# Kernel tuning notes

Measured on AMD Instinct MI355X. Metric: run time of the kernel, lower is better.

The kernel has to match this reference:

```python
import jax, jax.numpy as jnp
import numpy as np

B, S, HID = 4, 1024, 1024
H = 16
D = HID // H  # 64
SPARSITY = 0.9  # keep prob = 0.1


def setup_inputs() -> dict:
    key = jax.random.key(0)
    ks = jax.random.split(key, 11)
    sc = 1.0 / np.sqrt(HID)
    x = jax.random.normal(ks[0], (B, S, HID), dtype=jnp.float32)
    Wq = jax.random.normal(ks[1], (HID, HID), dtype=jnp.float32) * sc
    bq = jnp.zeros((HID,), dtype=jnp.float32)
    Wk = jax.random.normal(ks[2], (HID, HID), dtype=jnp.float32) * sc
    bk = jnp.zeros((HID,), dtype=jnp.float32)
    Wv = jax.random.normal(ks[3], (HID, HID), dtype=jnp.float32) * sc
    bv = jnp.zeros((HID,), dtype=jnp.float32)
    Wo = jax.random.normal(ks[4], (HID, HID), dtype=jnp.float32) * sc
    bo = jnp.zeros((HID,), dtype=jnp.float32)
    temperature = jnp.ones((H, 1, 1), dtype=jnp.float32)
    # training-mode random sparsity mask: rand > sparsity -> keep (True)
    sparse_mask = jax.random.uniform(ks[5], (B, H, S, S)) > SPARSITY
    return {"x": x, "Wq": Wq, "bq": bq, "Wk": Wk, "bk": bk, "Wv": Wv,
            "bv": bv, "Wo": Wo, "bo": bo, "temperature": temperature,
            "sparse_mask": sparse_mask}


def reference(x, Wq, bq, Wk, bk, Wv, bv, Wo, bo, temperature, sparse_mask):
    b, s, _ = x.shape
    def split_heads(t):
        return t.reshape(b, s, H, D).transpose(0, 2, 1, 3)  # [B,H,S,D]
    q = split_heads(x @ Wq + bq)
    k = split_heads(x @ Wk + bk)
    v = split_heads(x @ Wv + bv)
    scores = jnp.einsum('bhqd,bhkd->bhqk', q, k) / np.sqrt(D)
    scores = scores * temperature  # [H,1,1] broadcasts over [B,H,S,S]
    scores = jnp.where(sparse_mask, scores, -jnp.inf)
    attn = jax.nn.softmax(scores, axis=-1)
    out = jnp.einsum('bhqk,bhkd->bhqd', attn, v)
    out = out.transpose(0, 2, 1, 3).reshape(b, s, HID)
    return out @ Wo + bo
```

## Files before the change

### kernel.cpp

```cpp
#include <hip/hip_runtime.h>

typedef unsigned short u16;
typedef short short8 __attribute__((ext_vector_type(8)));
typedef float f32x4 __attribute__((ext_vector_type(4)));
typedef float float4v __attribute__((ext_vector_type(4)));
typedef u16 u16x4 __attribute__((ext_vector_type(4)));
typedef unsigned uint2v __attribute__((ext_vector_type(2)));
typedef unsigned long long u64;

__device__ __forceinline__ u16 f2bf(float f) {
  union { float f; unsigned u; } v; v.f = f;
  unsigned r = v.u + 0x7FFFu + ((v.u >> 16) & 1u);
  return (u16)(r >> 16);
}

__device__ __forceinline__ unsigned cvtpk(float lo, float hi) {
  unsigned r;
  asm("v_cvt_pk_bf16_f32 %0, %1, %2" : "=v"(r) : "v"(lo), "v"(hi));
  return r;
}

__device__ __forceinline__ void gload16(const u16* g, u16* l) {
  __builtin_amdgcn_global_load_lds(
      (const __attribute__((address_space(1))) void*)g,
      (__attribute__((address_space(3))) void*)l, 16, 0, 0);
}

union PackSS { unsigned u[4]; short8 s; };

__global__ __launch_bounds__(256)
void prep_kernel(const void* __restrict__ mask, u64* __restrict__ bits,
                 const float* __restrict__ x, u16* __restrict__ xb,
                 const float* __restrict__ W0, const float* __restrict__ W1,
                 const float* __restrict__ W2, const float* __restrict__ W3,
                 u16* __restrict__ Wt) {
  __shared__ float t[32][33];
  __shared__ int sf;
  const int bid = blockIdx.x;
  if (bid < 4096) {
    if (threadIdx.x == 0) sf = 0;
    __syncthreads();
    {
      uint4 v = ((const uint4*)mask)[threadIdx.x];
      unsigned xs[4] = {v.x, v.y, v.z, v.w};
      int f = 0;
#pragma unroll
      for (int d = 0; d < 4; ++d) {
        unsigned u = xs[d];
        if (u == 0x3F800000u) f |= 1;
        if (u & 0xFFFFFF00u) f |= 2;
        if ((d & 1) && u) f |= 4;
      }
      if (f) atomicOr(&sf, f);
    }
    __syncthreads();
    const int fl = sf;
    const int fmt = (fl & 1) ? 2 : ((fl & 2) ? 0 : ((fl & 4) ? 1 : 3));

    const int wi = bid * 256 + threadIdx.x;
    u64 b = 0;
    if (fmt == 0) {
      const uint4* mp = (const uint4*)mask + (size_t)wi * 4;
#pragma unroll
      for (int i = 0; i < 4; ++i) {
        uint4 v = mp[i];
        unsigned xw[4] = {v.x, v.y, v.z, v.w};
#pragma unroll
        for (int d = 0; d < 4; ++d)
#pragma unroll
          for (int by = 0; by < 4; ++by)
            if (xw[d] & (0xFFu << (by * 8))) b |= 1ULL << (i * 16 + d * 4 + by);
      }
    } else if (fmt != 3) {
      const uint4* mp = (const uint4*)mask + (size_t)wi * 16;
#pragma unroll
      for (int i = 0; i < 16; ++i) {
        uint4 v = mp[i];
        if (v.x) b |= 1ULL << (i * 4 + 0);
        if (v.y) b |= 1ULL << (i * 4 + 1);
        if (v.z) b |= 1ULL << (i * 4 + 2);
        if (v.w) b |= 1ULL << (i * 4 + 3);
      }
    } else {
      const uint4* mp = (const uint4*)mask + (size_t)wi * 32;
#pragma unroll
      for (int i = 0; i < 32; ++i) {
        uint4 v = mp[i];
        if (v.x | v.y) b |= 1ULL << (i * 2 + 0);
        if (v.z | v.w) b |= 1ULL << (i * 2 + 1);
      }
    }
    int bh = wi >> 14, q = (wi >> 4) & 1023, kt = wi & 15;
    bits[((size_t)bh * 16 + kt) * 1024 + q] = b;
  } else if (bid < 8192) {
    int i = ((bid - 4096) * 256 + threadIdx.x) * 4;
    float4v v = *(const float4v*)(x + i);
    u16x4 o;
    o[0] = f2bf(v[0]); o[1] = f2bf(v[1]); o[2] = f2bf(v[2]); o[3] = f2bf(v[3]);
    *(u16x4*)(xb + i) = o;
  } else {
    int i = bid - 8192;
    int z = i >> 10, rest = i & 1023;
    const float* W = (z == 0) ? W0 : (z == 1) ? W1 : (z == 2) ? W2 : W3;
    u16* out = Wt + (size_t)z * 1024 * 1024;
    int n0 = (rest & 31) * 32, k0 = (rest >> 5) * 32;
    int tx = threadIdx.x & 31, ty = threadIdx.x >> 5;
#pragma unroll
    for (int j = 0; j < 4; ++j)
      t[ty + 8 * j][tx] = W[(size_t)(k0 + ty + 8 * j) * 1024 + n0 + tx];
    __syncthreads();
#pragma unroll
    for (int j = 0; j < 4; ++j)
      out[(size_t)(n0 + ty + 8 * j) * 1024 + k0 + tx] = f2bf(t[tx][ty + 8 * j]);
  }
}

template<int BN>
__global__ __launch_bounds__(256)
void gemm_kernel(const u16* __restrict__ A,
                 const u16* __restrict__ Bt0, const u16* __restrict__ Bt1, const u16* __restrict__ Bt2,
                 const float* __restrict__ b0, const float* __restrict__ b1, const float* __restrict__ b2,
                 const float* __restrict__ temp,
                 u16* __restrict__ qb, u16* __restrict__ kb, u16* __restrict__ vT,
                 float* __restrict__ fo, int phase) {
  constexpr int K = 1024;
  constexpr int WN = BN / 2;
  constexpr int NC = WN / 16;
  __shared__ u16 As[128 * 32];
  __shared__ u16 Bs[BN * 32];
  const int tid = threadIdx.x;
  const int lane = tid & 63, w = tid >> 6;
  const int l15 = lane & 15, l4 = lane >> 4;
  const int m0 = blockIdx.x * 128, n0 = blockIdx.y * BN;
  const int z = blockIdx.z;
  const u16* Bt = (z == 0) ? Bt0 : (z == 1) ? Bt1 : Bt2;
  const float* bias = (z == 0) ? b0 : (z == 1) ? b1 : b2;
  const int wr = w >> 1, wc = w & 1;

  f32x4 acc[4][NC] = {};

  const int c0 = tid, c1 = 256 + tid;
  const u16* ga0 = A + (size_t)(m0 + (c0 >> 2)) * K + (c0 & 3) * 8;
  const u16* ga1 = A + (size_t)(m0 + (c1 >> 2)) * K + (c1 & 3) * 8;
  const u16* gb0 = Bt + (size_t)(n0 + (c0 >> 2)) * K + (c0 & 3) * 8;
  const u16* gb1 = Bt + (size_t)(n0 + (c1 >> 2)) * K + (c1 & 3) * 8;
  u16* la0 = As + c0 * 8;
  u16* la1 = As + c1 * 8;
  u16* lb0 = Bs + c0 * 8;
  u16* lb1 = Bs + c1 * 8;

  for (int kt = 0; kt < K; kt += 32) {
    gload16(ga0 + kt, la0);
    gload16(ga1 + kt, la1);
    gload16(gb0 + kt, lb0);
    if (BN == 128) gload16(gb1 + kt, lb1);
    __syncthreads();
    short8 af[4], bfr[NC];
#pragma unroll
    for (int r = 0; r < 4; ++r)
      af[r] = *(const short8*)(As + (wr * 64 + r * 16 + l15) * 32 + l4 * 8);
#pragma unroll
    for (int c = 0; c < NC; ++c)
      bfr[c] = *(const short8*)(Bs + (wc * WN + c * 16 + l15) * 32 + l4 * 8);
#pragma unroll
    for (int r = 0; r < 4; ++r)
#pragma unroll
      for (int c = 0; c < NC; ++c)
        acc[r][c] = __builtin_amdgcn_mfma_f32_16x16x32_bf16(bfr[c], af[r], acc[r][c], 0, 0, 0);
    __syncthreads();
  }

  float bvj[NC][4];
#pragma unroll
  for (int c = 0; c < NC; ++c)
#pragma unroll
    for (int j = 0; j < 4; ++j)
      bvj[c][j] = bias[n0 + wc * WN + c * 16 + l4 * 4 + j];
  const float fac = (phase == 0 && z == 0)
      ? temp[(n0 + wc * WN) >> 6] * 0.18033688011112042f : 1.0f;

#pragma unroll
  for (int r = 0; r < 4; ++r) {
    const int mm = m0 + wr * 64 + r * 16 + l15;
    const int b = mm >> 10, s = mm & 1023;
#pragma unroll
    for (int c = 0; c < NC; ++c) {
      const int n = n0 + wc * WN + c * 16 + l4 * 4;
      if (phase == 1) {
        float4v o;
#pragma unroll
        for (int j = 0; j < 4; ++j) o[j] = acc[r][c][j] + bvj[c][j];
        *(float4v*)(fo + (size_t)mm * 1024 + n) = o;
      } else if (z == 2) {
#pragma unroll
        for (int j = 0; j < 4; ++j)
          vT[((size_t)b * 1024 + n + j) * 1024 + s] = f2bf(acc[r][c][j] + bvj[c][j]);
      } else {
        unsigned lo = cvtpk((acc[r][c][0] + bvj[c][0]) * fac, (acc[r][c][1] + bvj[c][1]) * fac);
        unsigned hi = cvtpk((acc[r][c][2] + bvj[c][2]) * fac, (acc[r][c][3] + bvj[c][3]) * fac);
        unsigned o2[2] = {lo, hi};
        int hh = n >> 6, d = n & 63;
        u16* dst = (z == 0) ? qb : kb;
        *(unsigned long long*)(dst + ((((size_t)b * 16 + hh) * 1024 + s) * 64 + d)) =
            *(unsigned long long*)o2;
      }
    }
  }
}

__global__ __launch_bounds__(512, 4)
void attn_kernel(const u16* __restrict__ qb, const u16* __restrict__ kb, const u16* __restrict__ vT,
                 const u64* __restrict__ mbits, u16* __restrict__ oh) {
  __shared__ u16 Ks[2][64 * 64];
  __shared__ u16 Vs[2][64 * 64];
  const int tid = threadIdx.x, lane = tid & 63, w = tid >> 6;
  const int l15 = lane & 15, l4 = lane >> 4;
  const int id = blockIdx.x;
  const int xcd = id & 7, sl = id >> 3;
  const int bh = xcd * 8 + (sl >> 3), qx = sl & 7;
  const int b = bh >> 4, h = bh & 15;
  const int q0 = qx * 128 + w * 16;
  const u16* qp = qb + ((size_t)bh * 1024 + q0) * 64;
  const u16* kp = kb + (size_t)bh * 1024 * 64;
  const u16* vp = vT + (size_t)bh * 64 * 1024;

  const int sr = tid >> 3, sc = ((tid & 7) ^ (sr & 7)) * 8;
  const int swz8 = (l15 & 7) << 3;
  const int vswz = l15 & 7;

  short8 qf0 = *(const short8*)(qp + (size_t)l15 * 64 + l4 * 8);
  short8 qf1 = *(const short8*)(qp + (size_t)l15 * 64 + 32 + l4 * 8);

  float m = -1e30f, l = 0.f;
  f32x4 oacc[4] = {};

  const u64* mb = mbits + (size_t)bh * 16 * 1024 + q0 + l15;
  u64 wcur = mb[0];

  gload16(kp + (size_t)sr * 64 + sc, &Ks[0][tid * 8]);
  gload16(vp + (size_t)sr * 1024 + sc, &Vs[0][tid * 8]);

  for (int t = 0; t < 16; ++t) {
    const int buf = t & 1;
    __syncthreads();

    if (t < 15) {
      const int k1 = (t + 1) * 64;
      gload16(kp + (size_t)(k1 + sr) * 64 + sc, &Ks[buf ^ 1][tid * 8]);
      gload16(vp + (size_t)sr * 1024 + k1 + sc, &Vs[buf ^ 1][tid * 8]);
    }
    u64 wnext = (t < 15) ? mb[(t + 1) * 1024] : 0ULL;

    f32x4 s[4] = {};
    __builtin_amdgcn_s_setprio(1);
#pragma unroll
    for (int cb = 0; cb < 4; ++cb) {
      const u16* kr = &Ks[buf][(cb * 16 + l15) * 64];
      short8 kf0 = *(const short8*)(kr + ((l4 * 8) ^ swz8));
      short8 kf1 = *(const short8*)(kr + ((32 + l4 * 8) ^ swz8));
      s[cb] = __builtin_amdgcn_mfma_f32_16x16x32_bf16(kf0, qf0, s[cb], 0, 0, 0);
      s[cb] = __builtin_amdgcn_mfma_f32_16x16x32_bf16(kf1, qf1, s[cb], 0, 0, 0);
    }
    __builtin_amdgcn_s_setprio(0);

    float mt = fmaxf(fmaxf(s[0][0], s[0][1]), fmaxf(s[0][2], s[0][3]));
#pragma unroll
    for (int cb = 1; cb < 4; ++cb)
      mt = fmaxf(mt, fmaxf(fmaxf(s[cb][0], s[cb][1]), fmaxf(s[cb][2], s[cb][3])));
    mt = fmaxf(mt, __shfl_xor(mt, 16));
    mt = fmaxf(mt, __shfl_xor(mt, 32));
    if (!__all(mt <= m + 8.f)) {
      float mnew = fmaxf(m, mt);
      float al = exp2f(m - mnew);
      l *= al;
#pragma unroll
      for (int db = 0; db < 4; ++db) oacc[db] *= al;
      m = mnew;
    }
    unsigned hws[4] = {(unsigned)wcur, (unsigned)(wcur >> 16),
                       (unsigned)(wcur >> 32), (unsigned)(wcur >> 48)};
    float rs = 0.f;
#pragma unroll
    for (int cb = 0; cb < 4; ++cb) {
#pragma unroll
      for (int j = 0; j < 4; ++j) {
        float p = exp2f(s[cb][j] - m);
        p = ((hws[cb] >> (l4 * 4 + j)) & 1) ? p : 0.f;
        rs += p;
        s[cb][j] = p;
      }
    }
    rs += __shfl_xor(rs, 16);
    rs += __shfl_xor(rs, 32);
    l += rs;

    PackSS pb0, pb1;
    pb0.u[0] = cvtpk(s[0][0], s[0][1]); pb0.u[1] = cvtpk(s[0][2], s[0][3]);
    pb0.u[2] = cvtpk(s[1][0], s[1][1]); pb0.u[3] = cvtpk(s[1][2], s[1][3]);
    pb1.u[0] = cvtpk(s[2][0], s[2][1]); pb1.u[1] = cvtpk(s[2][2], s[2][3]);
    pb1.u[2] = cvtpk(s[3][0], s[3][1]); pb1.u[3] = cvtpk(s[3][2], s[3][3]);

    __builtin_amdgcn_s_setprio(1);
#pragma unroll
    for (int kg = 0; kg < 2; ++kg) {
#pragma unroll
      for (int db = 0; db < 4; ++db) {
        const u16* vrow = &Vs[buf][(db * 16 + l15) * 64];
        const int e0 = (((4 * kg + (l4 >> 1)) ^ vswz) << 3) + (l4 & 1) * 4;
        const int e1 = (((4 * kg + 2 + (l4 >> 1)) ^ vswz) << 3) + (l4 & 1) * 4;
        uint2v v0 = *(const uint2v*)(vrow + e0);
        uint2v v1 = *(const uint2v*)(vrow + e1);
        PackSS vf;
        vf.u[0] = v0[0]; vf.u[1] = v0[1]; vf.u[2] = v1[0]; vf.u[3] = v1[1];
        oacc[db] = __builtin_amdgcn_mfma_f32_16x16x32_bf16(
            vf.s, kg ? pb1.s : pb0.s, oacc[db], 0, 0, 0);
      }
    }
    __builtin_amdgcn_s_setprio(0);
    wcur = wnext;
  }

  float rl = 1.f / l;
  u16* orow = oh + ((size_t)b * 1024 + q0 + l15) * 1024 + h * 64;
#pragma unroll
  for (int db = 0; db < 4; ++db) {
    unsigned a0 = cvtpk(oacc[db][0] * rl, oacc[db][1] * rl);
    unsigned a1 = cvtpk(oacc[db][2] * rl, oacc[db][3] * rl);
    unsigned oA[2] = {a0, a1};
    *(unsigned long long*)(orow + db * 16 + l4 * 4) = *(unsigned long long*)oA;
  }
}

extern "C" void kernel_launch(void* const* d_in, const int* in_sizes, int n_in,
                              void* d_out, int out_size, void* d_ws, size_t ws_size,
                              hipStream_t stream) {
  const float* x = (const float*)d_in[0];
  const float* Wq = (const float*)d_in[1];
  const float* bq = (const float*)d_in[2];
  const float* Wk = (const float*)d_in[3];
  const float* bk = (const float*)d_in[4];
  const float* Wv = (const float*)d_in[5];
  const float* bv = (const float*)d_in[6];
  const float* Wo = (const float*)d_in[7];
  const float* bo = (const float*)d_in[8];
  const float* temp = (const float*)d_in[9];
  const void* mask = (const void*)d_in[10];

  char* ws = (char*)d_ws;
  u16* xb = (u16*)(ws + 256);
  u16* Wt = xb + (size_t)4 * 1024 * 1024;
  u16* qbuf = Wt + (size_t)4 * 1024 * 1024;
  u16* kbuf = qbuf + (size_t)4 * 1024 * 1024;
  u16* vTb = kbuf + (size_t)4 * 1024 * 1024;
  u64* mbits = (u64*)(vTb + (size_t)4 * 1024 * 1024);
  u16* oh = xb;

  prep_kernel<<<12288, 256, 0, stream>>>(mask, mbits, x, xb, Wq, Wk, Wv, Wo, Wt);
  gemm_kernel<128><<<dim3(32, 8, 3), 256, 0, stream>>>(
      xb, Wt, Wt + 1024 * 1024, Wt + 2 * 1024 * 1024,
      bq, bk, bv, temp, qbuf, kbuf, vTb, nullptr, 0);
  attn_kernel<<<512, 512, 0, stream>>>(qbuf, kbuf, vTb, mbits, oh);
  gemm_kernel<64><<<dim3(32, 16, 1), 256, 0, stream>>>(
      oh, Wt + 3 * 1024 * 1024, nullptr, nullptr,
      bo, nullptr, nullptr, temp, nullptr, nullptr, nullptr, (float*)d_out, 1);
}
```

Baseline: 188.4 us.

## Process two 16-row query tiles per wave in attention to reuse K/V fragments

The attention kernel moves from 8 waves of 16 query rows each to 4 waves of 32 query rows each, with 256 threads per block. Each K fragment and V fragment read from LDS now feeds two MFMAs, one per query sub-tile, which halves LDS reads per unit of work and gives more independent MFMAs to interleave with softmax. Each thread now issues two async global-to-LDS loads per tile, and LDS offsets are precomputed outside the loop. The cost is roughly doubled accumulator and score registers per wave and fewer waves per block, which may reduce occupancy and latency hiding.

```diff
diff --git a/kernel.cpp b/kernel.cpp
--- a/kernel.cpp
+++ b/kernel.cpp
@@ -20,7 +20,7 @@
   return r;
 }
 
-__device__ __forceinline__ void gload16(const u16* g, u16* l) {
+__device__ __forceinline__ void gload16(const void* g, void* l) {
   __builtin_amdgcn_global_load_lds(
       (const __attribute__((address_space(1))) void*)g,
       (__attribute__((address_space(3))) void*)l, 16, 0, 0);
@@ -102,7 +102,7 @@
     int i = bid - 8192;
     int z = i >> 10, rest = i & 1023;
     const float* W = (z == 0) ? W0 : (z == 1) ? W1 : (z == 2) ? W2 : W3;
-    u16* out = Wt + (size_t)z * 1024 * 1024;
+    u16* out = Wt + (size_t)z * 1048576;
     int n0 = (rest & 31) * 32, k0 = (rest >> 5) * 32;
     int tx = threadIdx.x & 31, ty = threadIdx.x >> 5;
 #pragma unroll
@@ -208,37 +208,96 @@
   }
 }
 
-__global__ __launch_bounds__(512, 4)
-void attn_kernel(const u16* __restrict__ qb, const u16* __restrict__ kb, const u16* __restrict__ vT,
-                 const u64* __restrict__ mbits, u16* __restrict__ oh) {
+__device__ __forceinline__ void softmax_reg(f32x4* s, u64 wcur, float& m, float& l,
+                                            f32x4* oacc, int l4,
+                                            PackSS& p0, PackSS& p1) {
+  float mt = fmaxf(fmaxf(s[0][0], s[0][1]), fmaxf(s[0][2], s[0][3]));
+#pragma unroll
+  for (int cb = 1; cb < 4; ++cb)
+    mt = fmaxf(mt, fmaxf(fmaxf(s[cb][0], s[cb][1]), fmaxf(s[cb][2], s[cb][3])));
+  mt = fmaxf(mt, __shfl_xor(mt, 16));
+  mt = fmaxf(mt, __shfl_xor(mt, 32));
+  if (!__all(mt <= m + 8.f)) {
+    float mnew = fmaxf(m, mt);
+    float al = exp2f(m - mnew);
+    l *= al;
+#pragma unroll
+    for (int db = 0; db < 4; ++db) oacc[db] *= al;
+    m = mnew;
+  }
+  unsigned hws[4] = {(unsigned)wcur, (unsigned)(wcur >> 16),
+                     (unsigned)(wcur >> 32), (unsigned)(wcur >> 48)};
+  float rs = 0.f;
+#pragma unroll
+  for (int cb = 0; cb < 4; ++cb) {
+#pragma unroll
+    for (int j = 0; j < 4; ++j) {
+      float p = exp2f(s[cb][j] - m);
+      p = ((hws[cb] >> (l4 * 4 + j)) & 1) ? p : 0.f;
+      rs += p;
+      s[cb][j] = p;
+    }
+  }
+  rs += __shfl_xor(rs, 16);
+  rs += __shfl_xor(rs, 32);
+  l += rs;
+  p0.u[0] = cvtpk(s[0][0], s[0][1]); p0.u[1] = cvtpk(s[0][2], s[0][3]);
+  p0.u[2] = cvtpk(s[1][0], s[1][1]); p0.u[3] = cvtpk(s[1][2], s[1][3]);
+  p1.u[0] = cvtpk(s[2][0], s[2][1]); p1.u[1] = cvtpk(s[2][2], s[2][3]);
+  p1.u[2] = cvtpk(s[3][0], s[3][1]); p1.u[3] = cvtpk(s[3][2], s[3][3]);
+}
+
+__global__ __launch_bounds__(256, 3)
+void attn_kernel(const u16* __restrict__ qb, const u16* __restrict__ kb,
+                 const u16* __restrict__ vT, const u64* __restrict__ mbits,
+                 u16* __restrict__ oh) {
   __shared__ u16 Ks[2][64 * 64];
   __shared__ u16 Vs[2][64 * 64];
   const int tid = threadIdx.x, lane = tid & 63, w = tid >> 6;
   const int l15 = lane & 15, l4 = lane >> 4;
   const int id = blockIdx.x;
-  const int xcd = id & 7, sl = id >> 3;
-  const int bh = xcd * 8 + (sl >> 3), qx = sl & 7;
+  const int xcd = id & 7;
+  const int bh = xcd * 8 + ((id >> 3) & 7), qx = id >> 6;
   const int b = bh >> 4, h = bh & 15;
-  const int q0 = qx * 128 + w * 16;
+  const int q0 = qx * 128 + w * 32;
   const u16* qp = qb + ((size_t)bh * 1024 + q0) * 64;
   const u16* kp = kb + (size_t)bh * 1024 * 64;
   const u16* vp = vT + (size_t)bh * 64 * 1024;
 
-  const int sr = tid >> 3, sc = ((tid & 7) ^ (sr & 7)) * 8;
+  const int L0 = tid, L1 = tid + 256;
+  const int r0 = L0 >> 3, c0 = ((L0 & 7) ^ (r0 & 7)) * 8;
+  const int r1 = L1 >> 3, c1 = ((L1 & 7) ^ (r1 & 7)) * 8;
   const int swz8 = (l15 & 7) << 3;
   const int vswz = l15 & 7;
 
-  short8 qf0 = *(const short8*)(qp + (size_t)l15 * 64 + l4 * 8);
-  short8 qf1 = *(const short8*)(qp + (size_t)l15 * 64 + 32 + l4 * 8);
-
-  float m = -1e30f, l = 0.f;
-  f32x4 oacc[4] = {};
+  int koff[4], vr[4], ke0, ke1, ve[2][2];
+#pragma unroll
+  for (int cb = 0; cb < 4; ++cb) koff[cb] = (cb * 16 + l15) * 64;
+#pragma unroll
+  for (int db = 0; db < 4; ++db) vr[db] = (db * 16 + l15) * 64;
+  ke0 = (l4 * 8) ^ swz8;
+  ke1 = (32 + l4 * 8) ^ swz8;
+#pragma unroll
+  for (int kg = 0; kg < 2; ++kg) {
+    ve[kg][0] = (((4 * kg + (l4 >> 1)) ^ vswz) << 3) + (l4 & 1) * 4;
+    ve[kg][1] = (((4 * kg + 2 + (l4 >> 1)) ^ vswz) << 3) + (l4 & 1) * 4;
+  }
+
+  short8 qa0 = *(const short8*)(qp + (size_t)l15 * 64 + l4 * 8);
+  short8 qa1 = *(const short8*)(qp + (size_t)l15 * 64 + 32 + l4 * 8);
+  short8 qb0 = *(const short8*)(qp + (size_t)(16 + l15) * 64 + l4 * 8);
+  short8 qb1 = *(const short8*)(qp + (size_t)(16 + l15) * 64 + 32 + l4 * 8);
+
+  float mA = -1e30f, lA = 0.f, mB = -1e30f, lB = 0.f;
+  f32x4 oA[4] = {}, oB[4] = {};
 
   const u64* mb = mbits + (size_t)bh * 16 * 1024 + q0 + l15;
-  u64 wcur = mb[0];
-
-  gload16(kp + (size_t)sr * 64 + sc, &Ks[0][tid * 8]);
-  gload16(vp + (size_t)sr * 1024 + sc, &Vs[0][tid * 8]);
+  u64 wA = mb[0], wB = mb[16];
+
+  gload16(kp + (size_t)r0 * 64 + c0, &Ks[0][L0 * 8]);
+  gload16(kp + (size_t)r1 * 64 + c1, &Ks[0][L1 * 8]);
+  gload16(vp + (size_t)r0 * 1024 + c0, &Vs[0][L0 * 8]);
+  gload16(vp + (size_t)r1 * 1024 + c1, &Vs[0][L1 * 8]);
 
   for (int t = 0; t < 16; ++t) {
     const int buf = t & 1;
@@ -246,88 +305,64 @@
 
     if (t < 15) {
       const int k1 = (t + 1) * 64;
-      gload16(kp + (size_t)(k1 + sr) * 64 + sc, &Ks[buf ^ 1][tid * 8]);
-      gload16(vp + (size_t)sr * 1024 + k1 + sc, &Vs[buf ^ 1][tid * 8]);
-    }
-    u64 wnext = (t < 15) ? mb[(t + 1) * 1024] : 0ULL;
-
-    f32x4 s[4] = {};
+      gload16(kp + (size_t)(k1 + r0) * 64 + c0, &Ks[buf ^ 1][L0 * 8]);
+      gload16(kp + (size_t)(k1 + r1) * 64 + c1, &Ks[buf ^ 1][L1 * 8]);
+      gload16(vp + (size_t)r0 * 1024 + k1 + c0, &Vs[buf ^ 1][L0 * 8]);
+      gload16(vp + (size_t)r1 * 1024 + k1 + c1, &Vs[buf ^ 1][L1 * 8]);
+    }
+    u64 wAn = 0, wBn = 0;
+    if (t < 15) { wAn = mb[(t + 1) * 1024]; wBn = mb[(t + 1) * 1024 + 16]; }
+
+    const u16* kbase = Ks[buf];
+    f32x4 sa[4] = {}, sb[4] = {};
     __builtin_amdgcn_s_setprio(1);
 #pragma unroll
     for (int cb = 0; cb < 4; ++cb) {
-      const u16* kr = &Ks[buf][(cb * 16 + l15) * 64];
-      short8 kf0 = *(const short8*)(kr + ((l4 * 8) ^ swz8));
-      short8 kf1 = *(const short8*)(kr + ((32 + l4 * 8) ^ swz8));
-      s[cb] = __builtin_amdgcn_mfma_f32_16x16x32_bf16(kf0, qf0, s[cb], 0, 0, 0);
-      s[cb] = __builtin_amdgcn_mfma_f32_16x16x32_bf16(kf1, qf1, s[cb], 0, 0, 0);
+      short8 kf0 = *(const short8*)(kbase + koff[cb] + ke0);
+      short8 kf1 = *(const short8*)(kbase + koff[cb] + ke1);
+      sa[cb] = __builtin_amdgcn_mfma_f32_16x16x32_bf16(kf0, qa0, sa[cb], 0, 0, 0);
+      sa[cb] = __builtin_amdgcn_mfma_f32_16x16x32_bf16(kf1, qa1, sa[cb], 0, 0, 0);
+      sb[cb] = __builtin_amdgcn_mfma_f32_16x16x32_bf16(kf0, qb0, sb[cb], 0, 0, 0);
+      sb[cb] = __builtin_amdgcn_mfma_f32_16x16x32_bf16(kf1, qb1, sb[cb], 0, 0, 0);
     }
     __builtin_amdgcn_s_setprio(0);
 
-    float mt = fmaxf(fmaxf(s[0][0], s[0][1]), fmaxf(s[0][2], s[0][3]));
-#pragma unroll
-    for (int cb = 1; cb < 4; ++cb)
-      mt = fmaxf(mt, fmaxf(fmaxf(s[cb][0], s[cb][1]), fmaxf(s[cb][2], s[cb][3])));
-    mt = fmaxf(mt, __shfl_xor(mt, 16));
-    mt = fmaxf(mt, __shfl_xor(mt, 32));
-    if (!__all(mt <= m + 8.f)) {
-      float mnew = fmaxf(m, mt);
-      float al = exp2f(m - mnew);
-      l *= al;
-#pragma unroll
-      for (int db = 0; db < 4; ++db) oacc[db] *= al;
-      m = mnew;
-    }
-    unsigned hws[4] = {(unsigned)wcur, (unsigned)(wcur >> 16),
-                       (unsigned)(wcur >> 32), (unsigned)(wcur >> 48)};
-    float rs = 0.f;
-#pragma unroll
-    for (int cb = 0; cb < 4; ++cb) {
-#pragma unroll
-      for (int j = 0; j < 4; ++j) {
-        float p = exp2f(s[cb][j] - m);
-        p = ((hws[cb] >> (l4 * 4 + j)) & 1) ? p : 0.f;
-        rs += p;
-        s[cb][j] = p;
-      }
-    }
-    rs += __shfl_xor(rs, 16);
-    rs += __shfl_xor(rs, 32);
-    l += rs;
-
-    PackSS pb0, pb1;
-    pb0.u[0] = cvtpk(s[0][0], s[0][1]); pb0.u[1] = cvtpk(s[0][2], s[0][3]);
-    pb0.u[2] = cvtpk(s[1][0], s[1][1]); pb0.u[3] = cvtpk(s[1][2], s[1][3]);
-    pb1.u[0] = cvtpk(s[2][0], s[2][1]); pb1.u[1] = cvtpk(s[2][2], s[2][3]);
-    pb1.u[2] = cvtpk(s[3][0], s[3][1]); pb1.u[3] = cvtpk(s[3][2], s[3][3]);
-
+    PackSS pa0, pa1, pb0, pb1;
+    softmax_reg(sa, wA, mA, lA, oA, l4, pa0, pa1);
+    softmax_reg(sb, wB, mB, lB, oB, l4, pb0, pb1);
+
+    const u16* vbase = Vs[buf];
     __builtin_amdgcn_s_setprio(1);
 #pragma unroll
     for (int kg = 0; kg < 2; ++kg) {
 #pragma unroll
       for (int db = 0; db < 4; ++db) {
-        const u16* vrow = &Vs[buf][(db * 16 + l15) * 64];
-        const int e0 = (((4 * kg + (l4 >> 1)) ^ vswz) << 3) + (l4 & 1) * 4;
-        const int e1 = (((4 * kg + 2 + (l4 >> 1)) ^ vswz) << 3) + (l4 & 1) * 4;
-        uint2v v0 = *(const uint2v*)(vrow + e0);
-        uint2v v1 = *(const uint2v*)(vrow + e1);
+        uint2v v0 = *(const uint2v*)(vbase + vr[db] + ve[kg][0]);
+        uint2v v1 = *(const uint2v*)(vbase + vr[db] + ve[kg][1]);
         PackSS vf;
         vf.u[0] = v0[0]; vf.u[1] = v0[1]; vf.u[2] = v1[0]; vf.u[3] = v1[1];
-        oacc[db] = __builtin_amdgcn_mfma_f32_16x16x32_bf16(
-            vf.s, kg ? pb1.s : pb0.s, oacc[db], 0, 0, 0);
+        oA[db] = __builtin_amdgcn_mfma_f32_16x16x32_bf16(
+            vf.s, kg ? pa1.s : pa0.s, oA[db], 0, 0, 0);
+        oB[db] = __builtin_amdgcn_mfma_f32_16x16x32_bf16(
+            vf.s, kg ? pb1.s : pb0.s, oB[db], 0, 0, 0);
       }
     }
     __builtin_amdgcn_s_setprio(0);
-    wcur = wnext;
-  }
-
-  float rl = 1.f / l;
-  u16* orow = oh + ((size_t)b * 1024 + q0 + l15) * 1024 + h * 64;
+    wA = wAn; wB = wBn;
+  }
+
+  float rlA = 1.f / lA, rlB = 1.f / lB;
+  u16* orowA = oh + ((size_t)b * 1024 + q0 + l15) * 1024 + h * 64;
+  u16* orowB = oh + ((size_t)b * 1024 + q0 + 16 + l15) * 1024 + h * 64;
 #pragma unroll
   for (int db = 0; db < 4; ++db) {
-    unsigned a0 = cvtpk(oacc[db][0] * rl, oacc[db][1] * rl);
-    unsigned a1 = cvtpk(oacc[db][2] * rl, oacc[db][3] * rl);
-    unsigned oA[2] = {a0, a1};
-    *(unsigned long long*)(orow + db * 16 + l4 * 4) = *(unsigned long long*)oA;
+    unsigned a0 = cvtpk(oA[db][0] * rlA, oA[db][1] * rlA);
+    unsigned a1 = cvtpk(oA[db][2] * rlA, oA[db][3] * rlA);
+    unsigned b0 = cvtpk(oB[db][0] * rlB, oB[db][1] * rlB);
+    unsigned b1 = cvtpk(oB[db][2] * rlB, oB[db][3] * rlB);
+    unsigned oAa[2] = {a0, a1}, oBb[2] = {b0, b1};
+    *(unsigned long long*)(orowA + db * 16 + l4 * 4) = *(unsigned long long*)oAa;
+    *(unsigned long long*)(orowB + db * 16 + l4 * 4) = *(unsigned long long*)oBb;
   }
 }
 
@@ -357,10 +392,10 @@
 
   prep_kernel<<<12288, 256, 0, stream>>>(mask, mbits, x, xb, Wq, Wk, Wv, Wo, Wt);
   gemm_kernel<128><<<dim3(32, 8, 3), 256, 0, stream>>>(
-      xb, Wt, Wt + 1024 * 1024, Wt + 2 * 1024 * 1024,
+      xb, Wt, Wt + 1048576, Wt + 2 * 1048576,
       bq, bk, bv, temp, qbuf, kbuf, vTb, nullptr, 0);
-  attn_kernel<<<512, 512, 0, stream>>>(qbuf, kbuf, vTb, mbits, oh);
+  attn_kernel<<<512, 256, 0, stream>>>(qbuf, kbuf, vTb, mbits, oh);
   gemm_kernel<64><<<dim3(32, 16, 1), 256, 0, stream>>>(
-      oh, Wt + 3 * 1024 * 1024, nullptr, nullptr,
+      oh, Wt + 3 * 1048576, nullptr, nullptr,
       bo, nullptr, nullptr, temp, nullptr, nullptr, nullptr, (float*)d_out, 1);
 }
```

Measured after the change: 190.1 us. About the same (+0.9%).
